# Kernel tuning notes

Measured on AMD Instinct MI355X. Metric: run time of the kernel, lower is better.

The kernel has to match this reference:

```python
import jax, jax.numpy as jnp
import numpy as np


@jax.custom_vjp
def spike(u):
    # Surrogate_BP_Function.forward: u.ge(0).float()
    return (u >= 0).astype(u.dtype)

def _spike_fwd(u):
    return spike(u), u

def _spike_bwd(u, g):
    # backward: g * 0.3 * relu(1 - |u|) * 2
    return (g * 0.6 * jnp.maximum(1.0 - jnp.abs(u), 0.0),)

spike.defvjp(_spike_fwd, _spike_bwd)


def setup_inputs() -> dict:
    key = jax.random.key(0)
    ks = jax.random.split(key, 5)
    B, T, I, H = 64, 512, 256, 512
    x = jax.random.normal(ks[0], (B, T, I), jnp.float32)
    conv1_w = jax.random.normal(ks[1], (H, I, 3), jnp.float32) * 0.1
    conv1_b = jax.random.normal(ks[2], (H,), jnp.float32) * 0.1
    conv2_w = jax.random.normal(ks[3], (H, H, 3), jnp.float32) * 0.1
    conv2_b = jax.random.normal(ks[4], (H,), jnp.float32) * 0.1
    th1 = jnp.ones((), jnp.float32)
    th2 = jnp.ones((), jnp.float32)
    return {"x": x, "conv1_w": conv1_w, "conv1_b": conv1_b,
            "conv2_w": conv2_w, "conv2_b": conv2_b, "th1": th1, "th2": th2}


def reference(x, conv1_w, conv1_b, conv2_w, conv2_b, th1, th2):
    leak = 1.0  # leak_mem from __init__
    # Conv1d(k=3, pad=1) on a length-1 sequence uses only the center tap.
    W1 = conv1_w[:, :, 1]  # [H, I]
    W2 = conv2_w[:, :, 1]  # [H, H]
    B, T, _ = x.shape
    H = W1.shape[0]
    # Precompute input drive for layer 1 (depends only on x[t]).
    z1 = jnp.einsum('bti,hi->bth', x, W1) + conv1_b  # [B, T, H]

    def step(carry, z1_t):
        m1, m2 = carry
        m1 = leak * m1 + z1_t
        thr1 = m1 / th1 - 1.0
        s1 = spike(thr1)
        m1 = m1 - th1 * (thr1 > 0).astype(x.dtype)
        m2 = leak * m2 + s1 @ W2.T + conv2_b
        thr2 = m2 / th2 - 1.0
        s2 = spike(thr2)
        m2 = m2 - th2 * (thr2 > 0).astype(x.dtype)
        return (m1, m2), s2

    init = (jnp.zeros((B, H), x.dtype), jnp.zeros((B, H), x.dtype))
    _, out_t = jax.lax.scan(step, init, jnp.swapaxes(z1, 0, 1))  # [T, B, H]
    return jnp.swapaxes(out_t, 0, 1)  # [B, T, H]
```

## Files before the change

### kernel.cpp

```cpp
#include <hip/hip_runtime.h>

#define BATCH 64
#define TSTEPS 512
#define IDIM 256
#define HDIM 512
#define MROWS (BATCH * TSTEPS)
#define KZ HDIM

typedef __attribute__((address_space(1))) const void gvoid;
typedef __attribute__((address_space(3))) void lvoid;

__device__ __forceinline__ void gl2lds16(const void* g, void* l) {
    __builtin_amdgcn_global_load_lds((gvoid*)g, (lvoid*)l, 16, 0, 0);
}

__global__ void extract_weights(const float* __restrict__ c1w,
                                const float* __restrict__ c2w,
                                float* __restrict__ W1T,
                                float* __restrict__ W2T) {
    int tid = blockIdx.x * 256 + threadIdx.x;
    if (tid < IDIM * HDIM) {
        int i = tid >> 9;
        int h = tid & 511;
        W1T[tid] = c1w[(h * IDIM + i) * 3 + 1];
    }
    if (tid < HDIM * HDIM) {
        int h = tid >> 9;
        int j = tid & 511;
        W2T[tid] = c2w[(j * HDIM + h) * 3 + 1];
    }
    if (tid < HDIM) {
        W2T[HDIM * HDIM + tid] = 0.0f;
    }
}

#define BM 128
#define BN 128
#define BK 16

__global__ __launch_bounds__(256, 2) void gemm_f32(const float* __restrict__ A,
                                                   const float* __restrict__ BT,
                                                   const float* __restrict__ bias,
                                                   float* __restrict__ C,
                                                   int K, int addBias) {
    __shared__ __align__(16) float As[BK * BM];
    __shared__ __align__(16) float Bs[BK * BN];

    const int N = HDIM;
    int tid  = threadIdx.x;
    int lane = tid & 63;
    int wave = tid >> 6;
    int row0 = blockIdx.x * BM;
    int col0 = blockIdx.y * BN;
    int wm = (wave >> 1) * 64;
    int wn = (wave & 1) * 64;
    int mbase = wm + (lane >> 3) * 8;
    int nbase = wn + (lane & 7) * 8;

    float acc[8][8];
#pragma unroll
    for (int i = 0; i < 8; i++)
#pragma unroll
        for (int j = 0; j < 8; j++) acc[i][j] = 0.0f;

    int ar = tid >> 1;
    int ak = (tid & 1) * 8;
    const float* ap = A + (size_t)(row0 + ar) * K + ak;

    const char* bp = (const char*)(BT + (size_t)(tid >> 5) * N + col0) + (tid & 31) * 16;
    char* bld = (char*)Bs + tid * 16;
    const size_t bRow8 = (size_t)8 * N * sizeof(float);

    for (int k0 = 0; k0 < K; k0 += BK) {
        gl2lds16(bp, bld);
        gl2lds16(bp + bRow8, bld + 4096);
        float4 a0 = *(const float4*)(ap);
        float4 a1 = *(const float4*)(ap + 4);
        ap += BK;
        bp += (size_t)BK * N * sizeof(float);
        As[(ak + 0) * BM + ar] = a0.x;
        As[(ak + 1) * BM + ar] = a0.y;
        As[(ak + 2) * BM + ar] = a0.z;
        As[(ak + 3) * BM + ar] = a0.w;
        As[(ak + 4) * BM + ar] = a1.x;
        As[(ak + 5) * BM + ar] = a1.y;
        As[(ak + 6) * BM + ar] = a1.z;
        As[(ak + 7) * BM + ar] = a1.w;
        __syncthreads();

#pragma unroll
        for (int k = 0; k < BK; k++) {
            float4 av0 = *(const float4*)&As[k * BM + mbase];
            float4 av1 = *(const float4*)&As[k * BM + mbase + 4];
            float4 bv0 = *(const float4*)&Bs[k * BN + nbase];
            float4 bv1 = *(const float4*)&Bs[k * BN + nbase + 4];
            float a8[8] = {av0.x, av0.y, av0.z, av0.w, av1.x, av1.y, av1.z, av1.w};
            float b8[8] = {bv0.x, bv0.y, bv0.z, bv0.w, bv1.x, bv1.y, bv1.z, bv1.w};
#pragma unroll
            for (int i = 0; i < 8; i++)
#pragma unroll
                for (int j = 0; j < 8; j++)
                    acc[i][j] = fmaf(a8[i], b8[j], acc[i][j]);
        }
        __syncthreads();
    }

    float bb[8];
#pragma unroll
    for (int j = 0; j < 8; j++)
        bb[j] = addBias ? bias[col0 + nbase + j] : 0.0f;
#pragma unroll
    for (int i = 0; i < 8; i++) {
        int row = row0 + mbase + i;
        float4* cp = (float4*)&C[(size_t)row * N + col0 + nbase];
        cp[0] = (float4){acc[i][0] + bb[0], acc[i][1] + bb[1],
                         acc[i][2] + bb[2], acc[i][3] + bb[3]};
        cp[1] = (float4){acc[i][4] + bb[4], acc[i][5] + bb[5],
                         acc[i][6] + bb[6], acc[i][7] + bb[7]};
    }
}

__global__ void lif_scan1(const float* __restrict__ z1,
                          unsigned long long* __restrict__ masks,
                          const float* __restrict__ th_p) {
    int gtid = blockIdx.x * blockDim.x + threadIdx.x;
    int b = gtid >> 9;
    int h = gtid & 511;
    int lane = threadIdx.x & 63;
    int w = h >> 6;
    float th = *th_p;
    const float* zp = z1 + (size_t)b * TSTEPS * HDIM + h;
    unsigned long long* mp = masks + (size_t)b * TSTEPS * 8 + w;
    float m = 0.0f;
    float bufA[16], bufB[16];
#pragma unroll
    for (int i = 0; i < 16; i++) bufA[i] = zp[(size_t)i * HDIM];
    for (int t0 = 0; t0 < TSTEPS; t0 += 32) {
#pragma unroll
        for (int i = 0; i < 16; i++) bufB[i] = zp[(size_t)(t0 + 16 + i) * HDIM];
        {
#pragma unroll
            for (int i = 0; i < 16; i++) {
                m += bufA[i];
                float thr = m / th - 1.0f;
                unsigned long long bal = __ballot(thr >= 0.0f);
                if (lane == 0) mp[(size_t)(t0 + i) * 8] = bal;
                if (thr > 0.0f) m -= th;
            }
        }
        if (t0 + 32 < TSTEPS) {
#pragma unroll
            for (int i = 0; i < 16; i++) bufA[i] = zp[(size_t)(t0 + 32 + i) * HDIM];
        }
        {
#pragma unroll
            for (int i = 0; i < 16; i++) {
                m += bufB[i];
                float thr = m / th - 1.0f;
                unsigned long long bal = __ballot(thr >= 0.0f);
                if (lane == 0) mp[(size_t)(t0 + 16 + i) * 8] = bal;
                if (thr > 0.0f) m -= th;
            }
        }
    }
}

#define CH 4

__global__ __launch_bounds__(64, 1) void spmm_spikes(
        const unsigned long long* __restrict__ masks,
        const float* __restrict__ W2T,
        float* __restrict__ C) {
    __shared__ __align__(16) float stage[2][CH][HDIM];
    __shared__ __align__(16) unsigned short klist[520];
    int lane = threadIdx.x;
    int m = blockIdx.x;
    const unsigned long long* mrow = masks + (size_t)m * 8;

    unsigned long long wv[8];
#pragma unroll
    for (int c = 0; c < 8; c++) wv[c] = mrow[c];

    int cnt = 0;
#pragma unroll
    for (int c = 0; c < 8; c++) {
        unsigned long long bal = wv[c];
        int below = (int)__popcll(bal & ((1ull << lane) - 1ull));
        if ((bal >> lane) & 1ull)
            klist[cnt + below] = (unsigned short)((c << 6) | lane);
        cnt += (int)__popcll(bal);
    }
    int pad = (-cnt) & (CH - 1);
    if (lane < pad) klist[cnt + lane] = (unsigned short)KZ;
    cnt += pad;
    cnt = __builtin_amdgcn_readfirstlane(cnt);
    int nch = cnt >> 2;

    float4 s0 = {0.0f, 0.0f, 0.0f, 0.0f};
    float4 s1 = {0.0f, 0.0f, 0.0f, 0.0f};

#define STAGE(buf, ci)                                                      \
    {                                                                       \
        ushort4 kq_ = *(const ushort4*)(klist + ((ci) << 2));               \
        const float* g0_ = W2T + (size_t)kq_.x * HDIM + (lane << 2);        \
        const float* g1_ = W2T + (size_t)kq_.y * HDIM + (lane << 2);        \
        const float* g2_ = W2T + (size_t)kq_.z * HDIM + (lane << 2);        \
        const float* g3_ = W2T + (size_t)kq_.w * HDIM + (lane << 2);        \
        float* l_ = &stage[buf][0][0] + (lane << 2);                        \
        gl2lds16(g0_,       l_);                                            \
        gl2lds16(g0_ + 256, l_ + 256);                                      \
        gl2lds16(g1_,       l_ + 512);                                      \
        gl2lds16(g1_ + 256, l_ + 768);                                      \
        gl2lds16(g2_,       l_ + 1024);                                     \
        gl2lds16(g2_ + 256, l_ + 1280);                                     \
        gl2lds16(g3_,       l_ + 1536);                                     \
        gl2lds16(g3_ + 256, l_ + 1792);                                     \
    }

    if (nch > 0) {
        asm volatile("s_waitcnt vmcnt(0)" ::: "memory");
        __builtin_amdgcn_sched_barrier(0);
        STAGE(0, 0);
        int cur = 0;
        for (int c = 0; c < nch; c++) {
            if (c + 1 < nch) {
                STAGE(cur ^ 1, c + 1);
                __builtin_amdgcn_sched_barrier(0);
                asm volatile("s_waitcnt vmcnt(8)" ::: "memory");
            } else {
                __builtin_amdgcn_sched_barrier(0);
                asm volatile("s_waitcnt vmcnt(0)" ::: "memory");
            }
            __builtin_amdgcn_sched_barrier(0);
            const float* base = &stage[cur][0][0] + (lane << 3);
#pragma unroll
            for (int q = 0; q < CH; q++) {
                float4 w0 = *(const float4*)(base + q * HDIM);
                float4 w1 = *(const float4*)(base + q * HDIM + 4);
                s0.x += w0.x; s0.y += w0.y; s0.z += w0.z; s0.w += w0.w;
                s1.x += w1.x; s1.y += w1.y; s1.z += w1.z; s1.w += w1.w;
            }
            __builtin_amdgcn_sched_barrier(0);
            cur ^= 1;
        }
    }
#undef STAGE

    float4* cp = (float4*)(C + (size_t)m * HDIM + (lane << 3));
    cp[0] = s0;
    cp[1] = s1;
}

__global__ void lif_scan2(const float* __restrict__ raw,
                          const float* __restrict__ b2,
                          const float* __restrict__ th_p,
                          float* __restrict__ out) {
    int gtid = blockIdx.x * blockDim.x + threadIdx.x;
    int b = gtid >> 9;
    int j = gtid & 511;
    float th = *th_p;
    float bias = b2[j];
    const float* rp = raw + (size_t)b * TSTEPS * HDIM + j;
    float* op = out + (size_t)b * TSTEPS * HDIM + j;
    float m = 0.0f;
    float bufA[16], bufB[16];
#pragma unroll
    for (int i = 0; i < 16; i++) bufA[i] = rp[(size_t)i * HDIM];
    for (int t0 = 0; t0 < TSTEPS; t0 += 32) {
#pragma unroll
        for (int i = 0; i < 16; i++) bufB[i] = rp[(size_t)(t0 + 16 + i) * HDIM];
        {
            float ss[16];
#pragma unroll
            for (int i = 0; i < 16; i++) {
                m = (m + bufA[i]) + bias;
                float thr = m / th - 1.0f;
                ss[i] = (thr >= 0.0f) ? 1.0f : 0.0f;
                if (thr > 0.0f) m -= th;
            }
#pragma unroll
            for (int i = 0; i < 16; i++) op[(size_t)(t0 + i) * HDIM] = ss[i];
        }
        if (t0 + 32 < TSTEPS) {
#pragma unroll
            for (int i = 0; i < 16; i++) bufA[i] = rp[(size_t)(t0 + 32 + i) * HDIM];
        }
        {
            float ss[16];
#pragma unroll
            for (int i = 0; i < 16; i++) {
                m = (m + bufB[i]) + bias;
                float thr = m / th - 1.0f;
                ss[i] = (thr >= 0.0f) ? 1.0f : 0.0f;
                if (thr > 0.0f) m -= th;
            }
#pragma unroll
            for (int i = 0; i < 16; i++) op[(size_t)(t0 + 16 + i) * HDIM] = ss[i];
        }
    }
}

extern "C" void kernel_launch(void* const* d_in, const int* in_sizes, int n_in,
                              void* d_out, int out_size, void* d_ws, size_t ws_size,
                              hipStream_t stream) {
    const float* x    = (const float*)d_in[0];
    const float* c1w  = (const float*)d_in[1];
    const float* c1b  = (const float*)d_in[2];
    const float* c2w  = (const float*)d_in[3];
    const float* c2b  = (const float*)d_in[4];
    const float* th1  = (const float*)d_in[5];
    const float* th2  = (const float*)d_in[6];
    float* out = (float*)d_out;

    float* W1T  = (float*)d_ws;
    float* W2T  = W1T + IDIM * HDIM;
    float* bufA = W2T + (HDIM + 1) * HDIM;
    unsigned long long* masks = (unsigned long long*)(bufA + (size_t)MROWS * HDIM);

    extract_weights<<<(HDIM * HDIM + 255) / 256, 256, 0, stream>>>(c1w, c2w, W1T, W2T);

    {
        dim3 grid(MROWS / BM, HDIM / BN);
        gemm_f32<<<grid, 256, 0, stream>>>(x, W1T, c1b, bufA, IDIM, 1);
    }

    lif_scan1<<<MROWS / 64, 64, 0, stream>>>(bufA, masks, th1);

    spmm_spikes<<<MROWS, 64, 0, stream>>>(masks, W2T, bufA);

    lif_scan2<<<MROWS / 64, 64, 0, stream>>>(bufA, c2b, th2, out);
}
```

Before: 381.0 us.

## Process two spike rows per block in SpMM with a continuous prefetch pipeline

Each spmm_spikes block now handles two output rows. The two rows' active-index lists are concatenated so a single double-buffered global-to-LDS pipeline runs across both without draining at the row boundary. The next chunk is now staged only after the current buffer has been consumed, and the LDS read and output layout changes from 8 contiguous floats per lane to two 4-float halves. The intent is to halve block launches, amortise pipeline fill and drain, and avoid the former overwrite of the buffer being read. The cost is fewer blocks for parallelism and longer per-block serial work.

```diff
diff --git a/kernel.cpp b/kernel.cpp
--- a/kernel.cpp
+++ b/kernel.cpp
@@ -166,42 +166,66 @@
 }
 
 #define CH 4
+#define RPB 2
 
 __global__ __launch_bounds__(64, 1) void spmm_spikes(
         const unsigned long long* __restrict__ masks,
         const float* __restrict__ W2T,
         float* __restrict__ C) {
     __shared__ __align__(16) float stage[2][CH][HDIM];
-    __shared__ __align__(16) unsigned short klist[520];
+    __shared__ __align__(16) unsigned short klist[2 * HDIM];
     int lane = threadIdx.x;
-    int m = blockIdx.x;
-    const unsigned long long* mrow = masks + (size_t)m * 8;
-
-    unsigned long long wv[8];
-#pragma unroll
-    for (int c = 0; c < 8; c++) wv[c] = mrow[c];
-
-    int cnt = 0;
+    int m0 = blockIdx.x * RPB;
+    const unsigned long long* mrow = masks + (size_t)m0 * 8;
+
+    unsigned long long wv[16];
+#pragma unroll
+    for (int c = 0; c < 16; c++) wv[c] = mrow[c];
+
+    int cnt0 = 0;
 #pragma unroll
     for (int c = 0; c < 8; c++) {
         unsigned long long bal = wv[c];
         int below = (int)__popcll(bal & ((1ull << lane) - 1ull));
         if ((bal >> lane) & 1ull)
-            klist[cnt + below] = (unsigned short)((c << 6) | lane);
-        cnt += (int)__popcll(bal);
-    }
-    int pad = (-cnt) & (CH - 1);
-    if (lane < pad) klist[cnt + lane] = (unsigned short)KZ;
-    cnt += pad;
-    cnt = __builtin_amdgcn_readfirstlane(cnt);
-    int nch = cnt >> 2;
+            klist[cnt0 + below] = (unsigned short)((c << 6) | lane);
+        cnt0 += (int)__popcll(bal);
+    }
+    int pad0 = (-cnt0) & (CH - 1);
+    if (lane < pad0) klist[cnt0 + lane] = (unsigned short)KZ;
+    cnt0 += pad0;
+    cnt0 = __builtin_amdgcn_readfirstlane(cnt0);
+
+    int cnt1 = 0;
+#pragma unroll
+    for (int c = 0; c < 8; c++) {
+        unsigned long long bal = wv[8 + c];
+        int below = (int)__popcll(bal & ((1ull << lane) - 1ull));
+        if ((bal >> lane) & 1ull)
+            klist[cnt0 + cnt1 + below] = (unsigned short)((c << 6) | lane);
+        cnt1 += (int)__popcll(bal);
+    }
+    int pad1 = (-cnt1) & (CH - 1);
+    if (lane < pad1) klist[cnt0 + cnt1 + lane] = (unsigned short)KZ;
+    cnt1 += pad1;
+    cnt1 = __builtin_amdgcn_readfirstlane(cnt1);
+
+    int nch0 = cnt0 >> 2;
+    int tc = (cnt0 + cnt1) >> 2;
 
     float4 s0 = {0.0f, 0.0f, 0.0f, 0.0f};
     float4 s1 = {0.0f, 0.0f, 0.0f, 0.0f};
-
-#define STAGE(buf, ci)                                                      \
+    float* crow0 = C + (size_t)m0 * HDIM;
+    float* crow1 = crow0 + HDIM;
+
+    if (nch0 == 0) {
+        *(float4*)(crow0 + (lane << 2))       = s0;
+        *(float4*)(crow0 + 256 + (lane << 2)) = s1;
+    }
+
+#define STAGE(buf, g)                                                       \
     {                                                                       \
-        ushort4 kq_ = *(const ushort4*)(klist + ((ci) << 2));               \
+        ushort4 kq_ = *(const ushort4*)(klist + ((g) << 2));                \
         const float* g0_ = W2T + (size_t)kq_.x * HDIM + (lane << 2);        \
         const float* g1_ = W2T + (size_t)kq_.y * HDIM + (lane << 2);        \
         const float* g2_ = W2T + (size_t)kq_.z * HDIM + (lane << 2);        \
@@ -217,38 +241,41 @@
         gl2lds16(g3_ + 256, l_ + 1792);                                     \
     }
 
-    if (nch > 0) {
+    if (tc > 0) {
         asm volatile("s_waitcnt vmcnt(0)" ::: "memory");
         __builtin_amdgcn_sched_barrier(0);
         STAGE(0, 0);
-        int cur = 0;
-        for (int c = 0; c < nch; c++) {
-            if (c + 1 < nch) {
-                STAGE(cur ^ 1, c + 1);
-                __builtin_amdgcn_sched_barrier(0);
+        if (tc > 1) STAGE(1, 1);
+        for (int g = 0; g < tc; g++) {
+            __builtin_amdgcn_sched_barrier(0);
+            if (g + 1 < tc) {
                 asm volatile("s_waitcnt vmcnt(8)" ::: "memory");
             } else {
-                __builtin_amdgcn_sched_barrier(0);
                 asm volatile("s_waitcnt vmcnt(0)" ::: "memory");
             }
             __builtin_amdgcn_sched_barrier(0);
-            const float* base = &stage[cur][0][0] + (lane << 3);
+            const float* base = &stage[g & 1][0][0] + (lane << 2);
 #pragma unroll
             for (int q = 0; q < CH; q++) {
                 float4 w0 = *(const float4*)(base + q * HDIM);
-                float4 w1 = *(const float4*)(base + q * HDIM + 4);
+                float4 w1 = *(const float4*)(base + q * HDIM + 256);
                 s0.x += w0.x; s0.y += w0.y; s0.z += w0.z; s0.w += w0.w;
                 s1.x += w1.x; s1.y += w1.y; s1.z += w1.z; s1.w += w1.w;
             }
             __builtin_amdgcn_sched_barrier(0);
-            cur ^= 1;
+            if (g == nch0 - 1) {
+                *(float4*)(crow0 + (lane << 2))       = s0;
+                *(float4*)(crow0 + 256 + (lane << 2)) = s1;
+                s0 = (float4){0.0f, 0.0f, 0.0f, 0.0f};
+                s1 = (float4){0.0f, 0.0f, 0.0f, 0.0f};
+            }
+            if (g + 2 < tc) STAGE(g & 1, g + 2);
         }
     }
 #undef STAGE
 
-    float4* cp = (float4*)(C + (size_t)m * HDIM + (lane << 3));
-    cp[0] = s0;
-    cp[1] = s1;
+    *(float4*)(crow1 + (lane << 2))       = s0;
+    *(float4*)(crow1 + 256 + (lane << 2)) = s1;
 }
 
 __global__ void lif_scan2(const float* __restrict__ raw,
@@ -326,7 +353,7 @@
 
     lif_scan1<<<MROWS / 64, 64, 0, stream>>>(bufA, masks, th1);
 
-    spmm_spikes<<<MROWS, 64, 0, stream>>>(masks, W2T, bufA);
+    spmm_spikes<<<MROWS / RPB, 64, 0, stream>>>(masks, W2T, bufA);
 
     lif_scan2<<<MROWS / 64, 64, 0, stream>>>(bufA, c2b, th2, out);
 }
```

After: 397.4 us. 4.3% more time.
